# Kernel optimization log

Hardware: AMD Instinct MI355X
Metric: run time of the kernel (lower is better)

The kernel has to match this reference:

```python
import jax, jax.numpy as jnp
import numpy as np

N_SINKHORN_ITERS = 20
SINKHORN_EPS = 1e-08  # also used as eps for the dynamic-H RMS norm (per docstring)
RMSNORM_EPS = 1e-05
ALPHA_INIT = 0.01
B, N_STREAMS, C = 4096, 4, 4096


def sinkhorn_knopp(M, num_iters=N_SINKHORN_ITERS, eps=SINKHORN_EPS):
    # Iterative row/column normalization toward a doubly-stochastic matrix.
    def body(i, M):
        M = M / (jnp.sum(M, axis=-1, keepdims=True) + eps)
        M = M / (jnp.sum(M, axis=-2, keepdims=True) + eps)
        return M
    return jax.lax.fori_loop(0, num_iters, body, M)


def setup_inputs() -> dict:
    key = jax.random.key(0)
    ks = jax.random.split(key, 4)
    n, nC = N_STREAMS, N_STREAMS * C
    return {
        "x": jax.random.normal(ks[0], (B, n, C), dtype=jnp.float32),
        "rmsnorm_weight": jnp.ones((C,), dtype=jnp.float32),
        "phi_pre": jax.random.normal(ks[1], (n, nC), dtype=jnp.float32) * 0.02,
        "phi_post": jax.random.normal(ks[2], (n, nC), dtype=jnp.float32) * 0.02,
        "phi_res": jax.random.normal(ks[3], (n * n, nC), dtype=jnp.float32) * 0.02,
        "b_pre": jnp.zeros((n,), dtype=jnp.float32),
        "b_post": jnp.zeros((n,), dtype=jnp.float32),
        "b_res": jnp.zeros((n, n), dtype=jnp.float32),
        "alpha_pre": jnp.float32(ALPHA_INIT),
        "alpha_post": jnp.float32(ALPHA_INIT),
        "alpha_res": jnp.float32(ALPHA_INIT),
    }


def reference(x, rmsnorm_weight, phi_pre, phi_post, phi_res,
              b_pre, b_post, b_res, alpha_pre, alpha_post, alpha_res):
    Bd, n, Cd = x.shape
    # --- dynamic H projections from RMS-normalized flattened streams ---
    xf = x.reshape(Bd, n * Cd)                                   # [B, nC]
    xn = xf * jax.lax.rsqrt(jnp.mean(xf * xf, axis=-1, keepdims=True) + SINKHORN_EPS)
    h_pre = alpha_pre * (xn @ phi_pre.T) + b_pre                 # [B, n]
    h_post = alpha_post * (xn @ phi_post.T) + b_post             # [B, n]
    h_res = (alpha_res * (xn @ phi_res.T)).reshape(Bd, n, n) + b_res  # [B, n, n]
    # --- manifold constraints ---
    H_pre = jax.nn.softmax(h_pre, axis=-1)                       # simplex (aggregation weights)
    H_post = 2.0 * jax.nn.sigmoid(h_post)                        # gain in (0, 2), ~1 at init
    M = sinkhorn_knopp(jnp.exp(h_res))                           # doubly-stochastic mixing [B, n, n]
    # --- aggregate -> rmsnorm -> distribute + mix + add ---
    x_agg = jnp.einsum('bn,bnc->bc', H_pre, x)                   # [B, C]
    y_norm = x_agg * jax.lax.rsqrt(jnp.mean(x_agg * x_agg, axis=-1, keepdims=True) + RMSNORM_EPS)
    y_norm = y_norm * rmsnorm_weight
    out = H_post[..., None] * y_norm[:, None, :] + jnp.einsum('bij,bjc->bic', M, x)
    return out
```

## Files before the change

### kernel.cpp

```cpp
#include <hip/hip_runtime.h>
#include <math.h>

#define B_ROWS 4096
#define NSTR 4
#define C_DIM 4096
#define NC 16384
#define NC4 4096
#define C4 1024

#define ASYNC_COPY16(g, l)                                                     \
    __builtin_amdgcn_global_load_lds(                                         \
        (const __attribute__((address_space(1))) void*)(g),                   \
        (__attribute__((address_space(3))) void*)(l), 16, 0, 0)

__global__ void repack_kernel(
    const float4* __restrict__ pre4,
    const float4* __restrict__ post4,
    const float4* __restrict__ res4,
    float4* __restrict__ phiws4)
{
    const int idx = blockIdx.x * blockDim.x + threadIdx.x;
    if (idx >= 24 * NC4) return;
    const int row = idx / NC4;
    const int k4  = idx % NC4;
    float4 v;
    if (row < 4)        v = pre4[row * NC4 + k4];
    else if (row < 8)   v = post4[(row - 4) * NC4 + k4];
    else                v = res4[(row - 8) * NC4 + k4];
    phiws4[idx] = v;
}

__global__ __launch_bounds__(256, 4) void proj_kernel(
    const float* __restrict__ x,
    const float* __restrict__ phiws,
    float* __restrict__ dots_part)
{
    const float4* __restrict__ x4   = reinterpret_cast<const float4*>(x);
    const float4* __restrict__ phi4 = reinterpret_cast<const float4*>(phiws);

    const int bid  = blockIdx.x;
    const int kb   = bid & 1;
    const int b0   = (bid >> 1) * 8;
    const int wave = threadIdx.x >> 6;
    const int lane = threadIdx.x & 63;
    const int wv   = __builtin_amdgcn_readfirstlane(wave);
    const int wr0  = 2 * wv;
    const int wr1  = 2 * wv + 1;

    __shared__ float4 xs[2][8][128];
    __shared__ float  red[4][8][6];
    __shared__ float  redss[8];

    const int kbase = kb * 2048;

    const float4* __restrict__ srcA = x4 + (size_t)(b0 + 2 * wave)     * NC4 + kbase + lane;
    const float4* __restrict__ srcB = x4 + (size_t)(b0 + 2 * wave + 1) * NC4 + kbase + lane;
    const float4* __restrict__ phibase = phi4 + (size_t)(wave * 6) * NC4 + kbase + lane;

    float acc[8][6];
#pragma unroll
    for (int r = 0; r < 8; ++r)
#pragma unroll
        for (int j = 0; j < 6; ++j) acc[r][j] = 0.f;
    float ssq0 = 0.f, ssq1 = 0.f;

    ASYNC_COPY16(srcA,      &xs[0][2 * wave][0]);
    ASYNC_COPY16(srcA + 64, &xs[0][2 * wave][64]);
    ASYNC_COPY16(srcB,      &xs[0][2 * wave + 1][0]);
    ASYNC_COPY16(srcB + 64, &xs[0][2 * wave + 1][64]);
    __syncthreads();

    int cur = 0;
#pragma unroll 1
    for (int c = 0; c < 16; ++c) {
        if (c < 15) {
            const int nf = (c + 1) * 128;
            ASYNC_COPY16(srcA + nf,      &xs[cur ^ 1][2 * wave][0]);
            ASYNC_COPY16(srcA + nf + 64, &xs[cur ^ 1][2 * wave][64]);
            ASYNC_COPY16(srcB + nf,      &xs[cur ^ 1][2 * wave + 1][0]);
            ASYNC_COPY16(srcB + nf + 64, &xs[cur ^ 1][2 * wave + 1][64]);
        }

        const float4* __restrict__ pb = phibase + c * 128;
#pragma unroll 1
        for (int u = 0; u < 2; ++u) {
            const int ki = u * 64 + lane;

            float4 p[6];
#pragma unroll
            for (int j = 0; j < 6; ++j)
                p[j] = pb[(size_t)j * NC4 + u * 64];

#pragma unroll
            for (int r = 0; r < 8; ++r) {
                const float4 xv = xs[cur][r][ki];
#pragma unroll
                for (int j = 0; j < 6; ++j) {
                    float a = acc[r][j];
                    a = fmaf(xv.x, p[j].x, a);
                    a = fmaf(xv.y, p[j].y, a);
                    a = fmaf(xv.z, p[j].z, a);
                    a = fmaf(xv.w, p[j].w, a);
                    acc[r][j] = a;
                }
                if (r == wr0) {
                    ssq0 = fmaf(xv.x, xv.x, ssq0);
                    ssq0 = fmaf(xv.y, xv.y, ssq0);
                    ssq0 = fmaf(xv.z, xv.z, ssq0);
                    ssq0 = fmaf(xv.w, xv.w, ssq0);
                } else if (r == wr1) {
                    ssq1 = fmaf(xv.x, xv.x, ssq1);
                    ssq1 = fmaf(xv.y, xv.y, ssq1);
                    ssq1 = fmaf(xv.z, xv.z, ssq1);
                    ssq1 = fmaf(xv.w, xv.w, ssq1);
                }
            }
        }

        __syncthreads();
        cur ^= 1;
    }

#pragma unroll
    for (int r = 0; r < 8; ++r)
#pragma unroll
        for (int j = 0; j < 6; ++j) {
            float v = acc[r][j];
#pragma unroll
            for (int off = 32; off > 0; off >>= 1)
                v += __shfl_xor(v, off, 64);
            acc[r][j] = v;
        }
#pragma unroll
    for (int off = 32; off > 0; off >>= 1)
        ssq0 += __shfl_xor(ssq0, off, 64);
#pragma unroll
    for (int off = 32; off > 0; off >>= 1)
        ssq1 += __shfl_xor(ssq1, off, 64);

    if (lane == 0) {
#pragma unroll
        for (int r = 0; r < 8; ++r)
#pragma unroll
            for (int j = 0; j < 6; ++j)
                red[wave][r][j] = acc[r][j];
        redss[2 * wave]     = ssq0;
        redss[2 * wave + 1] = ssq1;
    }
    __syncthreads();

    const int t = threadIdx.x;
    if (t < 200) {
        const int r = t / 25, o = t % 25;
        float s;
        if (o < 24) s = red[o / 6][r][o % 6];
        else        s = redss[r];
        dots_part[((size_t)kb * B_ROWS + (b0 + r)) * 25 + o] = s;
    }
}

__global__ void finalize_kernel(
    const float* __restrict__ dots_part,
    const float* __restrict__ b_pre,
    const float* __restrict__ b_post,
    const float* __restrict__ b_res,
    const float* __restrict__ alpha_pre,
    const float* __restrict__ alpha_post,
    const float* __restrict__ alpha_res,
    float* __restrict__ params)
{
    const int row = blockIdx.x * blockDim.x + threadIdx.x;
    if (row >= B_ROWS) return;

    const float* d0 = dots_part + (size_t)row * 25;
    const float* d1 = dots_part + ((size_t)B_ROWS + row) * 25;
    float d[25];
#pragma unroll
    for (int o = 0; o < 25; ++o) d[o] = d0[o] + d1[o];

    const float inv_rms = rsqrtf(d[24] * (1.f / (float)NC) + 1e-8f);
    const float ap  = alpha_pre[0];
    const float apo = alpha_post[0];
    const float ar  = alpha_res[0];

    float hp[4];
    float mx = -1e30f;
#pragma unroll
    for (int j = 0; j < 4; ++j) {
        hp[j] = ap * d[j] * inv_rms + b_pre[j];
        mx = fmaxf(mx, hp[j]);
    }
    float e[4], s = 0.f;
#pragma unroll
    for (int j = 0; j < 4; ++j) { e[j] = expf(hp[j] - mx); s += e[j]; }
    float Hpre[4];
#pragma unroll
    for (int j = 0; j < 4; ++j) Hpre[j] = e[j] / s;

    float Hpost[4];
#pragma unroll
    for (int j = 0; j < 4; ++j) {
        const float h = apo * d[4 + j] * inv_rms + b_post[j];
        Hpost[j] = 2.f / (1.f + expf(-h));
    }

    float M[16];
#pragma unroll
    for (int k = 0; k < 16; ++k)
        M[k] = expf(ar * d[8 + k] * inv_rms + b_res[k]);

    for (int it = 0; it < 20; ++it) {
#pragma unroll
        for (int i = 0; i < 4; ++i) {
            const float rs = M[i*4+0] + M[i*4+1] + M[i*4+2] + M[i*4+3] + 1e-8f;
#pragma unroll
            for (int j = 0; j < 4; ++j) M[i*4+j] = M[i*4+j] / rs;
        }
#pragma unroll
        for (int j = 0; j < 4; ++j) {
            const float cs = M[0*4+j] + M[1*4+j] + M[2*4+j] + M[3*4+j] + 1e-8f;
#pragma unroll
            for (int i = 0; i < 4; ++i) M[i*4+j] = M[i*4+j] / cs;
        }
    }

    float* p = params + (size_t)row * 24;
#pragma unroll
    for (int j = 0; j < 4; ++j)  p[j]     = Hpre[j];
#pragma unroll
    for (int j = 0; j < 4; ++j)  p[4 + j] = Hpost[j];
#pragma unroll
    for (int k = 0; k < 16; ++k) p[8 + k] = M[k];
}

__global__ __launch_bounds__(256, 2) void out_kernel(
    const float* __restrict__ x,
    const float* __restrict__ w,
    const float* __restrict__ params,
    float* __restrict__ out)
{
    const float4* __restrict__ x4 = reinterpret_cast<const float4*>(x);
    const float4* __restrict__ w4 = reinterpret_cast<const float4*>(w);
    float4* __restrict__ out4 = reinterpret_cast<float4*>(out);

    const int b = blockIdx.x;
    const float* __restrict__ p = params + (size_t)b * 24;

    float Hpre[4], Hpost[4], M[16];
#pragma unroll
    for (int j = 0; j < 4; ++j)  Hpre[j]  = p[j];
#pragma unroll
    for (int j = 0; j < 4; ++j)  Hpost[j] = p[4 + j];
#pragma unroll
    for (int k = 0; k < 16; ++k) M[k]     = p[8 + k];

    const int t = threadIdx.x;
    const size_t base = (size_t)b * NC4;

    float4 xv[4][4];
    float4 agg[4];
    float ssq = 0.f;

#pragma unroll
    for (int u = 0; u < 4; ++u) {
        const int c4 = u * 256 + t;
#pragma unroll
        for (int n = 0; n < 4; ++n)
            xv[u][n] = x4[base + (size_t)n * C4 + c4];

        float4 a;
        a.x = Hpre[0]*xv[u][0].x + Hpre[1]*xv[u][1].x + Hpre[2]*xv[u][2].x + Hpre[3]*xv[u][3].x;
        a.y = Hpre[0]*xv[u][0].y + Hpre[1]*xv[u][1].y + Hpre[2]*xv[u][2].y + Hpre[3]*xv[u][3].y;
        a.z = Hpre[0]*xv[u][0].z + Hpre[1]*xv[u][1].z + Hpre[2]*xv[u][2].z + Hpre[3]*xv[u][3].z;
        a.w = Hpre[0]*xv[u][0].w + Hpre[1]*xv[u][1].w + Hpre[2]*xv[u][2].w + Hpre[3]*xv[u][3].w;
        agg[u] = a;
        ssq += a.x*a.x + a.y*a.y + a.z*a.z + a.w*a.w;
    }

#pragma unroll
    for (int off = 32; off > 0; off >>= 1)
        ssq += __shfl_xor(ssq, off, 64);
    __shared__ float red[4];
    if ((t & 63) == 0) red[t >> 6] = ssq;
    __syncthreads();
    const float total = red[0] + red[1] + red[2] + red[3];
    const float inv = rsqrtf(total * (1.f / (float)C_DIM) + 1e-5f);

#pragma unroll
    for (int u = 0; u < 4; ++u) {
        const int c4 = u * 256 + t;
        const float4 wv = w4[c4];
        float4 y;
        y.x = agg[u].x * inv * wv.x;
        y.y = agg[u].y * inv * wv.y;
        y.z = agg[u].z * inv * wv.z;
        y.w = agg[u].w * inv * wv.w;

#pragma unroll
        for (int i = 0; i < 4; ++i) {
            float4 o;
            o.x = Hpost[i]*y.x + M[i*4+0]*xv[u][0].x + M[i*4+1]*xv[u][1].x
                               + M[i*4+2]*xv[u][2].x + M[i*4+3]*xv[u][3].x;
            o.y = Hpost[i]*y.y + M[i*4+0]*xv[u][0].y + M[i*4+1]*xv[u][1].y
                               + M[i*4+2]*xv[u][2].y + M[i*4+3]*xv[u][3].y;
            o.z = Hpost[i]*y.z + M[i*4+0]*xv[u][0].z + M[i*4+1]*xv[u][1].z
                               + M[i*4+2]*xv[u][2].z + M[i*4+3]*xv[u][3].z;
            o.w = Hpost[i]*y.w + M[i*4+0]*xv[u][0].w + M[i*4+1]*xv[u][1].w
                               + M[i*4+2]*xv[u][2].w + M[i*4+3]*xv[u][3].w;
            out4[base + (size_t)i * C4 + c4] = o;
        }
    }
}

extern "C" void kernel_launch(void* const* d_in, const int* in_sizes, int n_in,
                              void* d_out, int out_size, void* d_ws, size_t ws_size,
                              hipStream_t stream) {
    const float* x        = (const float*)d_in[0];
    const float* w        = (const float*)d_in[1];
    const float* phi_pre  = (const float*)d_in[2];
    const float* phi_post = (const float*)d_in[3];
    const float* phi_res  = (const float*)d_in[4];
    const float* b_pre    = (const float*)d_in[5];
    const float* b_post   = (const float*)d_in[6];
    const float* b_res    = (const float*)d_in[7];
    const float* a_pre    = (const float*)d_in[8];
    const float* a_post   = (const float*)d_in[9];
    const float* a_res    = (const float*)d_in[10];
    float* out = (float*)d_out;

    float* dots_part = (float*)d_ws;
    float* params    = dots_part + (size_t)2 * B_ROWS * 25;
    float* phiws     = params + (size_t)B_ROWS * 24;

    hipLaunchKernelGGL(repack_kernel, dim3((24 * NC4 + 255) / 256), dim3(256), 0, stream,
                       (const float4*)phi_pre, (const float4*)phi_post,
                       (const float4*)phi_res, (float4*)phiws);
    hipLaunchKernelGGL(proj_kernel, dim3(B_ROWS / 4), dim3(256), 0, stream,
                       x, phiws, dots_part);
    hipLaunchKernelGGL(finalize_kernel, dim3(B_ROWS / 256), dim3(256), 0, stream,
                       dots_part, b_pre, b_post, b_res, a_pre, a_post, a_res, params);
    hipLaunchKernelGGL(out_kernel, dim3(B_ROWS), dim3(256), 0, stream,
                       x, w, params, out);
}
```

Baseline: 217.7 us.

## Drop phi repack kernel and triple-buffer x chunks in proj kernel

Removes the separate repack kernel: proj_kernel now reads phi_pre/post/res directly through per-row base pointers, which saves a launch and a copy of the weights. The x staging changes from double-buffered 128-wide chunks to a triple-buffered ring of 64-wide chunks. Synchronisation uses explicit vmcnt waits and raw s_barrier with sched_barriers, so a prefetch two chunks ahead can stay in flight during compute. The hand-tuned waitcnt counts depend on the exact order of loads the compiler emits, so a miscount could produce a race.

Result: faster. 203.0 us (-6.7%).

```diff
diff --git a/kernel.cpp b/kernel.cpp
--- a/kernel.cpp
+++ b/kernel.cpp
@@ -13,30 +13,21 @@
         (const __attribute__((address_space(1))) void*)(g),                   \
         (__attribute__((address_space(3))) void*)(l), 16, 0, 0)
 
-__global__ void repack_kernel(
-    const float4* __restrict__ pre4,
-    const float4* __restrict__ post4,
-    const float4* __restrict__ res4,
-    float4* __restrict__ phiws4)
-{
-    const int idx = blockIdx.x * blockDim.x + threadIdx.x;
-    if (idx >= 24 * NC4) return;
-    const int row = idx / NC4;
-    const int k4  = idx % NC4;
-    float4 v;
-    if (row < 4)        v = pre4[row * NC4 + k4];
-    else if (row < 8)   v = post4[(row - 4) * NC4 + k4];
-    else                v = res4[(row - 8) * NC4 + k4];
-    phiws4[idx] = v;
-}
+#define DOT4(A, P, XV) { float _a = (A);                                       \
+    _a = fmaf((XV).x, (P).x, _a); _a = fmaf((XV).y, (P).y, _a);                \
+    _a = fmaf((XV).z, (P).z, _a); _a = fmaf((XV).w, (P).w, _a); (A) = _a; }
 
 __global__ __launch_bounds__(256, 4) void proj_kernel(
     const float* __restrict__ x,
-    const float* __restrict__ phiws,
+    const float* __restrict__ phi_pre,
+    const float* __restrict__ phi_post,
+    const float* __restrict__ phi_res,
     float* __restrict__ dots_part)
 {
-    const float4* __restrict__ x4   = reinterpret_cast<const float4*>(x);
-    const float4* __restrict__ phi4 = reinterpret_cast<const float4*>(phiws);
+    const float4* __restrict__ x4    = reinterpret_cast<const float4*>(x);
+    const float4* __restrict__ pre4  = reinterpret_cast<const float4*>(phi_pre);
+    const float4* __restrict__ post4 = reinterpret_cast<const float4*>(phi_post);
+    const float4* __restrict__ res4  = reinterpret_cast<const float4*>(phi_res);
 
     const int bid  = blockIdx.x;
     const int kb   = bid & 1;
@@ -47,15 +38,27 @@
     const int wr0  = 2 * wv;
     const int wr1  = 2 * wv + 1;
 
-    __shared__ float4 xs[2][8][128];
+    __shared__ float4 xs[3][8][64];
     __shared__ float  red[4][8][6];
     __shared__ float  redss[8];
 
     const int kbase = kb * 2048;
 
-    const float4* __restrict__ srcA = x4 + (size_t)(b0 + 2 * wave)     * NC4 + kbase + lane;
-    const float4* __restrict__ srcB = x4 + (size_t)(b0 + 2 * wave + 1) * NC4 + kbase + lane;
-    const float4* __restrict__ phibase = phi4 + (size_t)(wave * 6) * NC4 + kbase + lane;
+    const float4* srcA = x4 + (size_t)(b0 + 2 * wave)     * NC4 + kbase + lane;
+    const float4* srcB = x4 + (size_t)(b0 + 2 * wave + 1) * NC4 + kbase + lane;
+
+    const int row0 = wv * 6;
+    auto rowbase = [&](int row) -> const float4* {
+        if (row < 4)  return pre4  + (size_t)row * NC4;
+        if (row < 8)  return post4 + (size_t)(row - 4) * NC4;
+        return res4 + (size_t)(row - 8) * NC4;
+    };
+    const float4* pb0 = rowbase(row0 + 0) + kbase + lane;
+    const float4* pb1 = rowbase(row0 + 1) + kbase + lane;
+    const float4* pb2 = rowbase(row0 + 2) + kbase + lane;
+    const float4* pb3 = rowbase(row0 + 3) + kbase + lane;
+    const float4* pb4 = rowbase(row0 + 4) + kbase + lane;
+    const float4* pb5 = rowbase(row0 + 5) + kbase + lane;
 
     float acc[8][6];
 #pragma unroll
@@ -65,60 +68,54 @@
     float ssq0 = 0.f, ssq1 = 0.f;
 
     ASYNC_COPY16(srcA,      &xs[0][2 * wave][0]);
-    ASYNC_COPY16(srcA + 64, &xs[0][2 * wave][64]);
     ASYNC_COPY16(srcB,      &xs[0][2 * wave + 1][0]);
-    ASYNC_COPY16(srcB + 64, &xs[0][2 * wave + 1][64]);
-    __syncthreads();
-
-    int cur = 0;
+    ASYNC_COPY16(srcA + 64, &xs[1][2 * wave][0]);
+    ASYNC_COPY16(srcB + 64, &xs[1][2 * wave + 1][0]);
+    __builtin_amdgcn_sched_barrier(0);
+
+    int bc = 0;
+    int bf = 2;
+
 #pragma unroll 1
-    for (int c = 0; c < 16; ++c) {
-        if (c < 15) {
-            const int nf = (c + 1) * 128;
-            ASYNC_COPY16(srcA + nf,      &xs[cur ^ 1][2 * wave][0]);
-            ASYNC_COPY16(srcA + nf + 64, &xs[cur ^ 1][2 * wave][64]);
-            ASYNC_COPY16(srcB + nf,      &xs[cur ^ 1][2 * wave + 1][0]);
-            ASYNC_COPY16(srcB + nf + 64, &xs[cur ^ 1][2 * wave + 1][64]);
-        }
-
-        const float4* __restrict__ pb = phibase + c * 128;
-#pragma unroll 1
-        for (int u = 0; u < 2; ++u) {
-            const int ki = u * 64 + lane;
-
-            float4 p[6];
-#pragma unroll
-            for (int j = 0; j < 6; ++j)
-                p[j] = pb[(size_t)j * NC4 + u * 64];
-
-#pragma unroll
-            for (int r = 0; r < 8; ++r) {
-                const float4 xv = xs[cur][r][ki];
-#pragma unroll
-                for (int j = 0; j < 6; ++j) {
-                    float a = acc[r][j];
-                    a = fmaf(xv.x, p[j].x, a);
-                    a = fmaf(xv.y, p[j].y, a);
-                    a = fmaf(xv.z, p[j].z, a);
-                    a = fmaf(xv.w, p[j].w, a);
-                    acc[r][j] = a;
-                }
-                if (r == wr0) {
-                    ssq0 = fmaf(xv.x, xv.x, ssq0);
-                    ssq0 = fmaf(xv.y, xv.y, ssq0);
-                    ssq0 = fmaf(xv.z, xv.z, ssq0);
-                    ssq0 = fmaf(xv.w, xv.w, ssq0);
-                } else if (r == wr1) {
-                    ssq1 = fmaf(xv.x, xv.x, ssq1);
-                    ssq1 = fmaf(xv.y, xv.y, ssq1);
-                    ssq1 = fmaf(xv.z, xv.z, ssq1);
-                    ssq1 = fmaf(xv.w, xv.w, ssq1);
-                }
-            }
-        }
-
-        __syncthreads();
-        cur ^= 1;
+    for (int c = 0; c < 32; ++c) {
+        if (c == 0)       asm volatile("s_waitcnt vmcnt(2)" ::: "memory");
+        else if (c == 31) asm volatile("s_waitcnt vmcnt(0)" ::: "memory");
+        else              asm volatile("s_waitcnt vmcnt(8)" ::: "memory");
+        __builtin_amdgcn_sched_barrier(0);
+        __builtin_amdgcn_s_barrier();
+        __builtin_amdgcn_sched_barrier(0);
+
+        const float4 p0 = *pb0;
+        const float4 p1 = *pb1;
+        const float4 p2 = *pb2;
+        const float4 p3 = *pb3;
+        const float4 p4 = *pb4;
+        const float4 p5 = *pb5;
+        __builtin_amdgcn_sched_barrier(0);
+
+        if (c < 30) {
+            ASYNC_COPY16(srcA + 128, &xs[bf][2 * wave][0]);
+            ASYNC_COPY16(srcB + 128, &xs[bf][2 * wave + 1][0]);
+        }
+        __builtin_amdgcn_sched_barrier(0);
+
+#pragma unroll
+        for (int r = 0; r < 8; ++r) {
+            const float4 xv = xs[bc][r][lane];
+            DOT4(acc[r][0], p0, xv);
+            DOT4(acc[r][1], p1, xv);
+            DOT4(acc[r][2], p2, xv);
+            DOT4(acc[r][3], p3, xv);
+            DOT4(acc[r][4], p4, xv);
+            DOT4(acc[r][5], p5, xv);
+            if (r == wr0)      DOT4(ssq0, xv, xv)
+            else if (r == wr1) DOT4(ssq1, xv, xv)
+        }
+
+        srcA += 64; srcB += 64;
+        pb0 += 64; pb1 += 64; pb2 += 64; pb3 += 64; pb4 += 64; pb5 += 64;
+        bc = (bc == 2) ? 0 : bc + 1;
+        bf = (bf == 2) ? 0 : bf + 1;
     }
 
 #pragma unroll
@@ -330,13 +327,9 @@
 
     float* dots_part = (float*)d_ws;
     float* params    = dots_part + (size_t)2 * B_ROWS * 25;
-    float* phiws     = params + (size_t)B_ROWS * 24;
-
-    hipLaunchKernelGGL(repack_kernel, dim3((24 * NC4 + 255) / 256), dim3(256), 0, stream,
-                       (const float4*)phi_pre, (const float4*)phi_post,
-                       (const float4*)phi_res, (float4*)phiws);
+
     hipLaunchKernelGGL(proj_kernel, dim3(B_ROWS / 4), dim3(256), 0, stream,
-                       x, phiws, dots_part);
+                       x, phi_pre, phi_post, phi_res, dots_part);
     hipLaunchKernelGGL(finalize_kernel, dim3(B_ROWS / 256), dim3(256), 0, stream,
                        dots_part, b_pre, b_post, b_res, a_pre, a_post, a_res, params);
     hipLaunchKernelGGL(out_kernel, dim3(B_ROWS), dim3(256), 0, stream,
```
